# Kernel tuning notes

Measured on AMD Instinct MI355X. Metric: run time of the kernel, lower is better.

Reference implementation:

```python
import jax, jax.numpy as jnp
import numpy as np


def setup_inputs() -> dict:
    key = jax.random.key(0)
    ks = jax.random.split(key, 6)
    B, S, D, U = 32, 2048, 1024, 1024
    scale = 1.0 / np.sqrt(D)
    return {
        "h_enc": jax.random.normal(ks[0], (B, S, D), dtype=jnp.float32),
        "h_dec": jax.random.normal(ks[1], (B, D), dtype=jnp.float32),
        "W_enc": jax.random.normal(ks[2], (D, U), dtype=jnp.float32) * scale,
        "b_enc": jnp.zeros((U,), dtype=jnp.float32),
        "W_dec": jax.random.normal(ks[3], (D, U), dtype=jnp.float32) * scale,
        "b_dec": jnp.zeros((U,), dtype=jnp.float32),
        "W_com": jax.random.normal(ks[4], (U, 1), dtype=jnp.float32) * (1.0 / np.sqrt(U)),
        "b_com": jnp.zeros((1,), dtype=jnp.float32),
    }


def reference(h_enc, h_dec, W_enc, b_enc, W_dec, b_dec, W_com, b_com):
    # h_enc: [B,S,D] -> projected enc features [B,S,U]
    enc_p = jnp.einsum("bsd,du->bsu", h_enc, W_enc) + b_enc
    # h_dec: [B,D] -> [B,1,U]
    dec_p = (h_dec @ W_dec + b_dec)[:, None, :]
    # additive score: [B,S,1]
    score = jnp.einsum("bsu,uo->bso", jnp.tanh(dec_p + enc_p), W_com) + b_com
    attn = jax.nn.softmax(score, axis=1)  # softmax over seq axis
    # NOTE: original code multiplies attn by the PROJECTED h_enc (reassigned)
    context_vec = jnp.sum(attn * enc_p, axis=1)  # [B,U]
    return (context_vec, attn)
```

## Files before the change

### kernel.cpp

```cpp
#include <hip/hip_runtime.h>
#include <math.h>
#include <stdint.h>

#define Bz 32
#define Sz 2048
#define Dz 1024
#define Uz 1024
#define Mz (Bz*Sz)

typedef __attribute__((ext_vector_type(8))) short bf16x8;
typedef __attribute__((ext_vector_type(4))) float f32x4;

__device__ __forceinline__ unsigned short f2bf(float f) {
    union { float f; uint32_t u; } v; v.f = f;
    uint32_t r = v.u + 0x7FFFu + ((v.u >> 16) & 1u);
    return (unsigned short)(r >> 16);
}

__device__ __forceinline__ float fast_tanh(float x) {
    float e = __expf(2.f * x);
    return 1.f - 2.f * __builtin_amdgcn_rcpf(e + 1.f);
}

#define GLD16(gsrc, ldst) \
    __builtin_amdgcn_global_load_lds((__attribute__((address_space(1))) void*)(void*)(gsrc), \
        (__attribute__((address_space(3))) void*)(ldst), 16, 0, 0)

#define CONV_BLOCKS 16384
#define WT_BLOCKS   256
#define DECI_BLOCKS 32
#define SINIT_BLOCKS 64

__global__ __launch_bounds__(256) void prep_kernel(
    const float* __restrict__ h_enc, unsigned short* __restrict__ hbf,
    const float* __restrict__ W_enc, unsigned short* __restrict__ wT,
    const float* __restrict__ b_dec, float* __restrict__ dec_p,
    const float* __restrict__ b_com, float* __restrict__ score)
{
    __shared__ float tile[64][65];
    const int bid = blockIdx.x;
    const int tid = threadIdx.x;
    if (bid < CONV_BLOCKS) {
        const size_t i = ((size_t)bid * 256 + tid) * 16;
#pragma unroll
        for (int h = 0; h < 2; ++h) {
            const float4 a = *(const float4*)(h_enc + i + h * 8);
            const float4 c = *(const float4*)(h_enc + i + h * 8 + 4);
            union { unsigned short s[8]; uint4 v; } o;
            o.s[0] = f2bf(a.x); o.s[1] = f2bf(a.y); o.s[2] = f2bf(a.z); o.s[3] = f2bf(a.w);
            o.s[4] = f2bf(c.x); o.s[5] = f2bf(c.y); o.s[6] = f2bf(c.z); o.s[7] = f2bf(c.w);
            *(uint4*)(hbf + i + h * 8) = o.v;
        }
    } else if (bid < CONV_BLOCKS + WT_BLOCKS) {
        const int b2 = bid - CONV_BLOCKS;
        const int c  = tid & 63;
        const int r0 = tid >> 6;
        const int u0 = (b2 & 15) * 64;
        const int d0 = (b2 >> 4) * 64;
        for (int r = r0; r < 64; r += 4)
            tile[r][c] = W_enc[(size_t)(d0 + r) * Uz + u0 + c];
        __syncthreads();
        for (int r = r0; r < 64; r += 4)
            wT[(size_t)(u0 + r) * Dz + d0 + c] = f2bf(tile[c][r]);
    } else if (bid < CONV_BLOCKS + WT_BLOCKS + DECI_BLOCKS) {
        const int b3 = bid - (CONV_BLOCKS + WT_BLOCKS);
        const int u4 = tid * 4;
        *(float4*)&dec_p[b3 * Uz + u4] = *(const float4*)&b_dec[u4];
    } else {
        const int b4 = bid - (CONV_BLOCKS + WT_BLOCKS + DECI_BLOCKS);
        const float bc = b_com[0];
        const int i4 = (b4 * 256 + tid) * 4;
        float4 v = {bc, bc, bc, bc};
        *(float4*)&score[i4] = v;
    }
}

__global__ __launch_bounds__(256) void dec_partial_kernel(
    const float* __restrict__ h_dec, const float* __restrict__ W_dec,
    float* __restrict__ dec_p)
{
    __shared__ float hs[128];
    const int b  = blockIdx.x >> 3;
    const int d0 = (blockIdx.x & 7) * 128;
    const int tid = threadIdx.x;
    const int u4 = tid * 4;
    if (tid < 128) hs[tid] = h_dec[b * Dz + d0 + tid];
    __syncthreads();
    float4 acc = {0.f, 0.f, 0.f, 0.f};
#pragma unroll 4
    for (int d = 0; d < 128; ++d) {
        const float  a = hs[d];
        const float4 w = *(const float4*)&W_dec[(size_t)(d0 + d) * Uz + u4];
        acc.x += a * w.x; acc.y += a * w.y; acc.z += a * w.z; acc.w += a * w.w;
    }
    float* o = dec_p + b * Uz + u4;
    atomicAdd(o + 0, acc.x); atomicAdd(o + 1, acc.y);
    atomicAdd(o + 2, acc.z); atomicAdd(o + 3, acc.w);
}

__global__ __launch_bounds__(256) void score_mfma_kernel(
    const unsigned short* __restrict__ hbf,
    const unsigned short* __restrict__ wT,
    const float* __restrict__ dec_p,
    const float* __restrict__ W_com,
    float* __restrict__ score)
{
    __shared__ unsigned short As[8 * 512];
    __shared__ unsigned short Bs[8 * 512];

    const int tid  = threadIdx.x;
    const int w    = tid >> 6;
    const int lane = tid & 63;
    const int ln   = lane & 15;
    const int q    = lane >> 4;
    const int wm   = w & 1;
    const int wn   = w >> 1;
    const int m0   = (blockIdx.x >> 1) * 128;
    const int uh   = blockIdx.x & 1;
    const int b    = m0 / Sz;
    const int ub   = uh * 512;

    const int g0 = 2 * w;
    const unsigned short* a_src0 = hbf + (size_t)(m0 + g0 * 16 + ln) * Dz + q * 8;
    const unsigned short* a_src1 = a_src0 + (size_t)16 * Dz;
    unsigned short* a_dst0 = As + g0 * 512;
    unsigned short* a_dst1 = a_dst0 + 512;

    float racc[4][4];
#pragma unroll
    for (int i = 0; i < 4; ++i)
#pragma unroll
        for (int r = 0; r < 4; ++r) racc[i][r] = 0.f;

    for (int u0 = 0; u0 < 512; u0 += 128) {
        f32x4 acc[4][4];
#pragma unroll
        for (int i = 0; i < 4; ++i)
#pragma unroll
            for (int j = 0; j < 4; ++j) acc[i][j] = (f32x4){0.f, 0.f, 0.f, 0.f};

        const unsigned short* b_src0 = wT + (size_t)(ub + u0 + g0 * 16 + ln) * Dz + q * 8;
        const unsigned short* b_src1 = b_src0 + (size_t)16 * Dz;
        unsigned short* b_dst0 = Bs + g0 * 512;
        unsigned short* b_dst1 = b_dst0 + 512;

        for (int k0 = 0; k0 < Dz; k0 += 32) {
            __syncthreads();
            GLD16(a_src0 + k0, a_dst0);
            GLD16(a_src1 + k0, a_dst1);
            GLD16(b_src0 + k0, b_dst0);
            GLD16(b_src1 + k0, b_dst1);
            __syncthreads();

            bf16x8 af[4], bfr[4];
#pragma unroll
            for (int i = 0; i < 4; ++i)
                af[i] = *(const bf16x8*)(As + (wm * 4 + i) * 512 + lane * 8);
#pragma unroll
            for (int j = 0; j < 4; ++j)
                bfr[j] = *(const bf16x8*)(Bs + (wn * 4 + j) * 512 + lane * 8);
#pragma unroll
            for (int i = 0; i < 4; ++i)
#pragma unroll
                for (int j = 0; j < 4; ++j)
                    acc[i][j] = __builtin_amdgcn_mfma_f32_16x16x32_bf16(
                        af[i], bfr[j], acc[i][j], 0, 0, 0);
        }

        float dpv[4], wcv[4];
#pragma unroll
        for (int j = 0; j < 4; ++j) {
            const int u = ub + u0 + (wn * 4 + j) * 16 + ln;
            dpv[j] = dec_p[b * Uz + u];
            wcv[j] = W_com[u];
        }
#pragma unroll
        for (int i = 0; i < 4; ++i)
#pragma unroll
            for (int r = 0; r < 4; ++r) {
                float v = 0.f;
#pragma unroll
                for (int j = 0; j < 4; ++j)
                    v += fast_tanh(acc[i][j][r] + dpv[j]) * wcv[j];
                racc[i][r] += v;
            }
    }

#pragma unroll
    for (int off = 1; off < 16; off <<= 1)
#pragma unroll
        for (int i = 0; i < 4; ++i)
#pragma unroll
            for (int r = 0; r < 4; ++r)
                racc[i][r] += __shfl_xor(racc[i][r], off, 64);
    if (ln == 0) {
#pragma unroll
        for (int i = 0; i < 4; ++i)
#pragma unroll
            for (int r = 0; r < 4; ++r)
                atomicAdd(&score[m0 + wm * 64 + i * 16 + q * 4 + r], racc[i][r]);
    }
}

__global__ __launch_bounds__(256) void softmax_init_kernel(
    const float* __restrict__ score, float* __restrict__ attn,
    const float* __restrict__ b_enc, float* __restrict__ out_ctx,
    float* __restrict__ wsum)
{
    __shared__ float red[256];
    const int tid = threadIdx.x;
    if (blockIdx.x >= 2 * Bz) {
        const int b3 = blockIdx.x - 2 * Bz;
        float4 z = {0.f, 0.f, 0.f, 0.f};
        *(float4*)&wsum[b3 * Dz + tid * 4] = z;
        return;
    }
    if (blockIdx.x >= Bz) {
        const int b2 = blockIdx.x - Bz;
        const int u4 = tid * 4;
        *(float4*)&out_ctx[b2 * Uz + u4] = *(const float4*)&b_enc[u4];
        return;
    }
    const int b = blockIdx.x;
    const float* srow = score + b * Sz;
    float v[8];
    float lm = -1e30f;
#pragma unroll
    for (int i = 0; i < 8; ++i) { v[i] = srow[i * 256 + tid]; lm = fmaxf(lm, v[i]); }
    red[tid] = lm; __syncthreads();
    for (int off = 128; off > 0; off >>= 1) {
        if (tid < off) red[tid] = fmaxf(red[tid], red[tid + off]);
        __syncthreads();
    }
    const float mx = red[0];
    __syncthreads();
    float ls = 0.f;
#pragma unroll
    for (int i = 0; i < 8; ++i) { v[i] = expf(v[i] - mx); ls += v[i]; }
    red[tid] = ls; __syncthreads();
    for (int off = 128; off > 0; off >>= 1) {
        if (tid < off) red[tid] += red[tid + off];
        __syncthreads();
    }
    const float inv = 1.f / red[0];
#pragma unroll
    for (int i = 0; i < 8; ++i) attn[b * Sz + i * 256 + tid] = v[i] * inv;
}

__global__ __launch_bounds__(256) void wsum_kernel(
    const float* __restrict__ h_enc, const float* __restrict__ attn,
    float* __restrict__ wsum)
{
    __shared__ float aw[64];
    const int b  = blockIdx.x >> 5;
    const int s0 = (blockIdx.x & 31) * 64;
    const int tid = threadIdx.x;
    if (tid < 64) aw[tid] = attn[b * Sz + s0 + tid];
    __syncthreads();
    float4 acc = {0.f, 0.f, 0.f, 0.f};
    const float* base = h_enc + ((size_t)b * Sz + s0) * Dz + tid * 4;
#pragma unroll 4
    for (int s = 0; s < 64; ++s) {
        const float a = aw[s];
        const float4 h = *(const float4*)(base + (size_t)s * Dz);
        acc.x += a * h.x; acc.y += a * h.y; acc.z += a * h.z; acc.w += a * h.w;
    }
    float* o = wsum + b * Dz + tid * 4;
    atomicAdd(o + 0, acc.x); atomicAdd(o + 1, acc.y);
    atomicAdd(o + 2, acc.z); atomicAdd(o + 3, acc.w);
}

__global__ __launch_bounds__(256) void ctx_partial_kernel(
    const float* __restrict__ wsum, const float* __restrict__ W_enc,
    float* __restrict__ out_ctx)
{
    __shared__ float hs[128];
    const int b  = blockIdx.x >> 3;
    const int d0 = (blockIdx.x & 7) * 128;
    const int tid = threadIdx.x;
    const int u4 = tid * 4;
    if (tid < 128) hs[tid] = wsum[b * Dz + d0 + tid];
    __syncthreads();
    float4 acc = {0.f, 0.f, 0.f, 0.f};
#pragma unroll 4
    for (int d = 0; d < 128; ++d) {
        const float  a = hs[d];
        const float4 wv = *(const float4*)&W_enc[(size_t)(d0 + d) * Uz + u4];
        acc.x += a * wv.x; acc.y += a * wv.y; acc.z += a * wv.z; acc.w += a * wv.w;
    }
    float* o = out_ctx + b * Uz + u4;
    atomicAdd(o + 0, acc.x); atomicAdd(o + 1, acc.y);
    atomicAdd(o + 2, acc.z); atomicAdd(o + 3, acc.w);
}

__global__ __launch_bounds__(256) void dec_proj_kernel(
    const float* __restrict__ h_dec, const float* __restrict__ W_dec,
    const float* __restrict__ b_dec, float* __restrict__ dec_p)
{
    __shared__ float hs[Dz];
    const int b = blockIdx.x >> 2;
    const int u = ((blockIdx.x & 3) << 8) + threadIdx.x;
    for (int d = threadIdx.x; d < Dz; d += 256) hs[d] = h_dec[b * Dz + d];
    __syncthreads();
    float acc = 0.f;
#pragma unroll 4
    for (int d = 0; d < Dz; ++d) acc += hs[d] * W_dec[d * Uz + u];
    dec_p[b * Uz + u] = acc + b_dec[u];
}

#define MT 64
#define NT 64
#define KT 64
__global__ __launch_bounds__(256) void score_kernel(
    const float* __restrict__ h_enc, const float* __restrict__ W_enc,
    const float* __restrict__ dec_p, const float* __restrict__ W_com,
    const float* __restrict__ b_com, float* __restrict__ score)
{
    __shared__ __align__(16) float As[KT][MT + 4];
    __shared__ __align__(16) float Bs[KT][NT + 4];
    __shared__ float red[MT][17];
    const int tid = threadIdx.x;
    const int tx = tid & 15;
    const int ty = tid >> 4;
    const int m0 = blockIdx.x * MT;
    const int b  = m0 / Sz;
    float s_acc = 0.f;
    for (int u0 = 0; u0 < Uz; u0 += NT) {
        float acc[4][4];
#pragma unroll
        for (int i = 0; i < 4; ++i)
#pragma unroll
            for (int j = 0; j < 4; ++j) acc[i][j] = 0.f;
        for (int k0 = 0; k0 < Dz; k0 += KT) {
            __syncthreads();
#pragma unroll
            for (int i = 0; i < 4; ++i) {
                const int row = ty + i * 16;
                const int c4  = tx * 4;
                const float4 v = *(const float4*)&h_enc[(size_t)(m0 + row) * Dz + k0 + c4];
                As[c4 + 0][row] = v.x; As[c4 + 1][row] = v.y;
                As[c4 + 2][row] = v.z; As[c4 + 3][row] = v.w;
            }
#pragma unroll
            for (int i = 0; i < 4; ++i) {
                const int row = ty + i * 16;
                *(float4*)&Bs[row][tx * 4] =
                    *(const float4*)&W_enc[(size_t)(k0 + row) * Uz + u0 + tx * 4];
            }
            __syncthreads();
#pragma unroll 8
            for (int k = 0; k < KT; ++k) {
                const float4 a = *(const float4*)&As[k][ty * 4];
                const float4 wv = *(const float4*)&Bs[k][tx * 4];
                acc[0][0] += a.x * wv.x; acc[0][1] += a.x * wv.y; acc[0][2] += a.x * wv.z; acc[0][3] += a.x * wv.w;
                acc[1][0] += a.y * wv.x; acc[1][1] += a.y * wv.y; acc[1][2] += a.y * wv.z; acc[1][3] += a.y * wv.w;
                acc[2][0] += a.z * wv.x; acc[2][1] += a.z * wv.y; acc[2][2] += a.z * wv.z; acc[2][3] += a.z * wv.w;
                acc[3][0] += a.w * wv.x; acc[3][1] += a.w * wv.y; acc[3][2] += a.w * wv.z; acc[3][3] += a.w * wv.w;
            }
        }
        const float4 dp = *(const float4*)&dec_p[b * Uz + u0 + tx * 4];
        const float4 wc = *(const float4*)&W_com[u0 + tx * 4];
#pragma unroll
        for (int i = 0; i < 4; ++i) {
            const float p = tanhf(acc[i][0] + dp.x) * wc.x + tanhf(acc[i][1] + dp.y) * wc.y
                          + tanhf(acc[i][2] + dp.z) * wc.z + tanhf(acc[i][3] + dp.w) * wc.w;
            red[ty * 4 + i][tx] = p;
        }
        __syncthreads();
        if (tid < MT) {
            float t = 0.f;
#pragma unroll
            for (int j = 0; j < 16; ++j) t += red[tid][j];
            s_acc += t;
        }
    }
    if (tid < MT) score[m0 + tid] = s_acc + b_com[0];
}

__global__ __launch_bounds__(256) void ctx_kernel(
    const float* __restrict__ wsum, const float* __restrict__ W_enc,
    const float* __restrict__ b_enc, float* __restrict__ out)
{
    __shared__ float hs[Dz];
    const int b = blockIdx.x >> 2;
    const int u = ((blockIdx.x & 3) << 8) + threadIdx.x;
    for (int d = threadIdx.x; d < Dz; d += 256) hs[d] = wsum[b * Dz + d];
    __syncthreads();
    float acc = 0.f;
#pragma unroll 4
    for (int d = 0; d < Dz; ++d) acc += hs[d] * W_enc[d * Uz + u];
    out[b * Uz + u] = acc + b_enc[u];
}

extern "C" void kernel_launch(void* const* d_in, const int* in_sizes, int n_in,
                              void* d_out, int out_size, void* d_ws, size_t ws_size,
                              hipStream_t stream)
{
    const float* h_enc = (const float*)d_in[0];
    const float* h_dec = (const float*)d_in[1];
    const float* W_enc = (const float*)d_in[2];
    const float* b_enc = (const float*)d_in[3];
    const float* W_dec = (const float*)d_in[4];
    const float* b_dec = (const float*)d_in[5];
    const float* W_com = (const float*)d_in[6];
    const float* b_com = (const float*)d_in[7];

    float* out_ctx  = (float*)d_out;
    float* out_attn = out_ctx + Bz * Uz;

    const size_t HBF_BYTES = (size_t)Mz * Dz * 2;
    const size_t WT_BYTES  = (size_t)Uz * Dz * 2;
    const size_t SMALL     = (size_t)(Bz*Uz + Bz*Sz + Bz*Dz) * 4;
    const size_t need      = HBF_BYTES + WT_BYTES + SMALL;

    if (ws_size >= need) {
        char* wsb = (char*)d_ws;
        unsigned short* hbf = (unsigned short*)wsb;
        unsigned short* wT  = (unsigned short*)(wsb + HBF_BYTES);
        float* dec_p = (float*)(wsb + HBF_BYTES + WT_BYTES);
        float* score = dec_p + Bz * Uz;
        float* wsum  = score + Bz * Sz;

        prep_kernel<<<CONV_BLOCKS + WT_BLOCKS + DECI_BLOCKS + SINIT_BLOCKS, 256, 0, stream>>>(
            h_enc, hbf, W_enc, wT, b_dec, dec_p, b_com, score);
        dec_partial_kernel<<<Bz * 8, 256, 0, stream>>>(h_dec, W_dec, dec_p);
        score_mfma_kernel<<<(Mz / 128) * 2, 256, 0, stream>>>(hbf, wT, dec_p, W_com, score);
        softmax_init_kernel<<<3 * Bz, 256, 0, stream>>>(score, out_attn, b_enc, out_ctx, wsum);
        wsum_kernel<<<Bz * 32, 256, 0, stream>>>(h_enc, out_attn, wsum);
        ctx_partial_kernel<<<Bz * 8, 256, 0, stream>>>(wsum, W_enc, out_ctx);
    } else {
        float* ws    = (float*)d_ws;
        float* dec_p = ws;
        float* score = ws + Bz * Uz;
        float* wsum  = ws + Bz * Uz + Bz * Sz;

        dec_proj_kernel<<<(Bz * Uz) / 256, 256, 0, stream>>>(h_dec, W_dec, b_dec, dec_p);
        score_kernel<<<Mz / MT, 256, 0, stream>>>(h_enc, W_enc, dec_p, W_com, b_com, score);
        softmax_init_kernel<<<3 * Bz, 256, 0, stream>>>(score, out_attn, b_enc, out_ctx, wsum);
        wsum_kernel<<<Bz * 32, 256, 0, stream>>>(h_enc, out_attn, wsum);
        ctx_kernel<<<(Bz * Uz) / 256, 256, 0, stream>>>(wsum, W_enc, b_enc, out_ctx);
    }
}
```

Baseline: 763.8 us.

## Double MFMA K-tile depth and fold decoder projection into prep kernel

The score GEMM now stages a 64-wide K slice per barrier pair instead of 32, which halves the number of __syncthreads rounds and doubles the LDS tiles. Launch bounds are set to request 3 blocks per CU. The separate decoder-projection kernel with atomics is removed, and prep_kernel blocks compute dec_p directly, which saves one launch and the atomic traffic. The cost is more LDS per block, possible occupancy or register pressure, and a slower serial per-thread dot product for dec_p.

```diff
diff --git a/kernel.cpp b/kernel.cpp
--- a/kernel.cpp
+++ b/kernel.cpp
@@ -28,16 +28,18 @@
 
 #define CONV_BLOCKS 16384
 #define WT_BLOCKS   256
-#define DECI_BLOCKS 32
+#define DEC_BLOCKS  128
 #define SINIT_BLOCKS 64
 
 __global__ __launch_bounds__(256) void prep_kernel(
     const float* __restrict__ h_enc, unsigned short* __restrict__ hbf,
     const float* __restrict__ W_enc, unsigned short* __restrict__ wT,
+    const float* __restrict__ h_dec, const float* __restrict__ W_dec,
     const float* __restrict__ b_dec, float* __restrict__ dec_p,
     const float* __restrict__ b_com, float* __restrict__ score)
 {
     __shared__ float tile[64][65];
+    __shared__ float hs[Dz];
     const int bid = blockIdx.x;
     const int tid = threadIdx.x;
     if (bid < CONV_BLOCKS) {
@@ -62,12 +64,18 @@
         __syncthreads();
         for (int r = r0; r < 64; r += 4)
             wT[(size_t)(u0 + r) * Dz + d0 + c] = f2bf(tile[c][r]);
-    } else if (bid < CONV_BLOCKS + WT_BLOCKS + DECI_BLOCKS) {
+    } else if (bid < CONV_BLOCKS + WT_BLOCKS + DEC_BLOCKS) {
         const int b3 = bid - (CONV_BLOCKS + WT_BLOCKS);
-        const int u4 = tid * 4;
-        *(float4*)&dec_p[b3 * Uz + u4] = *(const float4*)&b_dec[u4];
+        const int b  = b3 >> 2;
+        const int u  = ((b3 & 3) << 8) + tid;
+        for (int d = tid; d < Dz; d += 256) hs[d] = h_dec[b * Dz + d];
+        __syncthreads();
+        float acc = 0.f;
+#pragma unroll 4
+        for (int d = 0; d < Dz; ++d) acc += hs[d] * W_dec[(size_t)d * Uz + u];
+        dec_p[b * Uz + u] = acc + b_dec[u];
     } else {
-        const int b4 = bid - (CONV_BLOCKS + WT_BLOCKS + DECI_BLOCKS);
+        const int b4 = bid - (CONV_BLOCKS + WT_BLOCKS + DEC_BLOCKS);
         const float bc = b_com[0];
         const int i4 = (b4 * 256 + tid) * 4;
         float4 v = {bc, bc, bc, bc};
@@ -75,38 +83,15 @@
     }
 }
 
-__global__ __launch_bounds__(256) void dec_partial_kernel(
-    const float* __restrict__ h_dec, const float* __restrict__ W_dec,
-    float* __restrict__ dec_p)
-{
-    __shared__ float hs[128];
-    const int b  = blockIdx.x >> 3;
-    const int d0 = (blockIdx.x & 7) * 128;
-    const int tid = threadIdx.x;
-    const int u4 = tid * 4;
-    if (tid < 128) hs[tid] = h_dec[b * Dz + d0 + tid];
-    __syncthreads();
-    float4 acc = {0.f, 0.f, 0.f, 0.f};
-#pragma unroll 4
-    for (int d = 0; d < 128; ++d) {
-        const float  a = hs[d];
-        const float4 w = *(const float4*)&W_dec[(size_t)(d0 + d) * Uz + u4];
-        acc.x += a * w.x; acc.y += a * w.y; acc.z += a * w.z; acc.w += a * w.w;
-    }
-    float* o = dec_p + b * Uz + u4;
-    atomicAdd(o + 0, acc.x); atomicAdd(o + 1, acc.y);
-    atomicAdd(o + 2, acc.z); atomicAdd(o + 3, acc.w);
-}
-
-__global__ __launch_bounds__(256) void score_mfma_kernel(
+__global__ __launch_bounds__(256, 3) void score_mfma_kernel(
     const unsigned short* __restrict__ hbf,
     const unsigned short* __restrict__ wT,
     const float* __restrict__ dec_p,
     const float* __restrict__ W_com,
     float* __restrict__ score)
 {
-    __shared__ unsigned short As[8 * 512];
-    __shared__ unsigned short Bs[8 * 512];
+    __shared__ unsigned short As[16 * 512];
+    __shared__ unsigned short Bs[16 * 512];
 
     const int tid  = threadIdx.x;
     const int w    = tid >> 6;
@@ -116,15 +101,15 @@
     const int wm   = w & 1;
     const int wn   = w >> 1;
     const int m0   = (blockIdx.x >> 1) * 128;
-    const int uh   = blockIdx.x & 1;
+    const int ub   = (blockIdx.x & 1) * 512;
     const int b    = m0 / Sz;
-    const int ub   = uh * 512;
-
-    const int g0 = 2 * w;
-    const unsigned short* a_src0 = hbf + (size_t)(m0 + g0 * 16 + ln) * Dz + q * 8;
-    const unsigned short* a_src1 = a_src0 + (size_t)16 * Dz;
-    unsigned short* a_dst0 = As + g0 * 512;
-    unsigned short* a_dst1 = a_dst0 + 512;
+
+    const unsigned short* a_srcA = hbf + (size_t)(m0 + (2 * w + 0) * 16 + ln) * Dz + q * 8;
+    const unsigned short* a_srcB = a_srcA + (size_t)16 * Dz;
+    unsigned short* a_dst0 = As + ((2 * w + 0) * 2 + 0) * 512;
+    unsigned short* a_dst1 = As + ((2 * w + 0) * 2 + 1) * 512;
+    unsigned short* a_dst2 = As + ((2 * w + 1) * 2 + 0) * 512;
+    unsigned short* a_dst3 = As + ((2 * w + 1) * 2 + 1) * 512;
 
     float racc[4][4];
 #pragma unroll
@@ -139,32 +124,41 @@
 #pragma unroll
             for (int j = 0; j < 4; ++j) acc[i][j] = (f32x4){0.f, 0.f, 0.f, 0.f};
 
-        const unsigned short* b_src0 = wT + (size_t)(ub + u0 + g0 * 16 + ln) * Dz + q * 8;
-        const unsigned short* b_src1 = b_src0 + (size_t)16 * Dz;
-        unsigned short* b_dst0 = Bs + g0 * 512;
-        unsigned short* b_dst1 = b_dst0 + 512;
-
-        for (int k0 = 0; k0 < Dz; k0 += 32) {
+        const unsigned short* b_srcA = wT + (size_t)(ub + u0 + (2 * w + 0) * 16 + ln) * Dz + q * 8;
+        const unsigned short* b_srcB = b_srcA + (size_t)16 * Dz;
+        unsigned short* b_dst0 = Bs + ((2 * w + 0) * 2 + 0) * 512;
+        unsigned short* b_dst1 = Bs + ((2 * w + 0) * 2 + 1) * 512;
+        unsigned short* b_dst2 = Bs + ((2 * w + 1) * 2 + 0) * 512;
+        unsigned short* b_dst3 = Bs + ((2 * w + 1) * 2 + 1) * 512;
+
+        for (int k0 = 0; k0 < Dz; k0 += 64) {
             __syncthreads();
-            GLD16(a_src0 + k0, a_dst0);
-            GLD16(a_src1 + k0, a_dst1);
-            GLD16(b_src0 + k0, b_dst0);
-            GLD16(b_src1 + k0, b_dst1);
+            GLD16(a_srcA + k0,      a_dst0);
+            GLD16(a_srcA + k0 + 32, a_dst1);
+            GLD16(a_srcB + k0,      a_dst2);
+            GLD16(a_srcB + k0 + 32, a_dst3);
+            GLD16(b_srcA + k0,      b_dst0);
+            GLD16(b_srcA + k0 + 32, b_dst1);
+            GLD16(b_srcB + k0,      b_dst2);
+            GLD16(b_srcB + k0 + 32, b_dst3);
             __syncthreads();
 
-            bf16x8 af[4], bfr[4];
-#pragma unroll
-            for (int i = 0; i < 4; ++i)
-                af[i] = *(const bf16x8*)(As + (wm * 4 + i) * 512 + lane * 8);
-#pragma unroll
-            for (int j = 0; j < 4; ++j)
-                bfr[j] = *(const bf16x8*)(Bs + (wn * 4 + j) * 512 + lane * 8);
-#pragma unroll
-            for (int i = 0; i < 4; ++i)
+#pragma unroll
+            for (int kg = 0; kg < 2; ++kg) {
+                bf16x8 af[4], bfr[4];
+#pragma unroll
+                for (int i = 0; i < 4; ++i)
+                    af[i] = *(const bf16x8*)(As + ((wm * 4 + i) * 2 + kg) * 512 + lane * 8);
 #pragma unroll
                 for (int j = 0; j < 4; ++j)
-                    acc[i][j] = __builtin_amdgcn_mfma_f32_16x16x32_bf16(
-                        af[i], bfr[j], acc[i][j], 0, 0, 0);
+                    bfr[j] = *(const bf16x8*)(Bs + ((wn * 4 + j) * 2 + kg) * 512 + lane * 8);
+#pragma unroll
+                for (int i = 0; i < 4; ++i)
+#pragma unroll
+                    for (int j = 0; j < 4; ++j)
+                        acc[i][j] = __builtin_amdgcn_mfma_f32_16x16x32_bf16(
+                            af[i], bfr[j], acc[i][j], 0, 0, 0);
+            }
         }
 
         float dpv[4], wcv[4];
@@ -421,9 +415,8 @@
         float* score = dec_p + Bz * Uz;
         float* wsum  = score + Bz * Sz;
 
-        prep_kernel<<<CONV_BLOCKS + WT_BLOCKS + DECI_BLOCKS + SINIT_BLOCKS, 256, 0, stream>>>(
-            h_enc, hbf, W_enc, wT, b_dec, dec_p, b_com, score);
-        dec_partial_kernel<<<Bz * 8, 256, 0, stream>>>(h_dec, W_dec, dec_p);
+        prep_kernel<<<CONV_BLOCKS + WT_BLOCKS + DEC_BLOCKS + SINIT_BLOCKS, 256, 0, stream>>>(
+            h_enc, hbf, W_enc, wT, h_dec, W_dec, b_dec, dec_p, b_com, score);
         score_mfma_kernel<<<(Mz / 128) * 2, 256, 0, stream>>>(hbf, wT, dec_p, W_com, score);
         softmax_init_kernel<<<3 * Bz, 256, 0, stream>>>(score, out_attn, b_enc, out_ctx, wsum);
         wsum_kernel<<<Bz * 32, 256, 0, stream>>>(h_enc, out_attn, wsum);
```

Result: slower. 840.7 us (+10.1%).
